# Kernel optimization log

Hardware: AMD Instinct MI355X
Metric: run time of the kernel (lower is better)

## Reference

```python
import jax, jax.numpy as jnp
import numpy as np

DIM = 256
N_PATCHES = 2048
N_HEADS = 8
BATCH = 2


def setup_inputs() -> dict:
    key = jax.random.key(0)
    ks = jax.random.split(key, 8)
    d = DIM
    s = d ** -0.5
    return {
        "x": jax.random.normal(ks[0], (BATCH, N_PATCHES, d), dtype=jnp.float32),
        # weights stored (in_features, out_features) so y = x @ W + b
        "W_qk": jax.random.normal(ks[1], (d, 2 * d), dtype=jnp.float32) * s,
        "W_v": jax.random.normal(ks[2], (d, d), dtype=jnp.float32) * s,
        "W_proj": jax.random.normal(ks[3], (d, d), dtype=jnp.float32) * s,
        "b_proj": jnp.zeros((d,), dtype=jnp.float32),
        "W_pos": jax.random.normal(ks[4], (2, N_HEADS), dtype=jnp.float32) * 0.5,
        "b_pos": jnp.zeros((N_HEADS,), dtype=jnp.float32),
        "gating": jnp.ones((N_HEADS,), dtype=jnp.float32),
    }


def reference(x, W_qk, W_v, W_proj, b_proj, W_pos, b_pos, gating):
    B, N, C = x.shape
    H = gating.shape[0]
    Dh = C // H
    scale = Dh ** -0.5

    # content attention: q @ k^T softmax
    qk = (x @ W_qk).reshape(B, N, 2, H, Dh)
    q = jnp.transpose(qk[:, :, 0], (0, 2, 1, 3))  # [B,H,N,Dh]
    k = jnp.transpose(qk[:, :, 1], (0, 2, 1, 3))
    patch_score = jax.nn.softmax(jnp.einsum("bhnd,bhmd->bhnm", q, k) * scale, axis=-1)

    # positional attention from relative indices (d, |d|) -> per-head score
    idx = jnp.arange(N, dtype=jnp.float32)
    rel = idx[:, None] - idx[None, :]                      # [N,N]
    rel_feat = jnp.stack([rel, jnp.abs(rel)], axis=-1)     # [N,N,2]
    pos = rel_feat @ W_pos + b_pos                         # [N,N,H]
    pos_score = jax.nn.softmax(jnp.transpose(pos, (2, 0, 1)), axis=-1)  # [H,N,N]

    g = jax.nn.sigmoid(gating)[None, :, None, None]        # [1,H,1,1]
    attn = (1.0 - g) * patch_score + g * pos_score[None]   # [B,H,N,N]
    attn = attn / jnp.sum(attn, axis=-1, keepdims=True)

    v = jnp.transpose((x @ W_v).reshape(B, N, H, Dh), (0, 2, 1, 3))  # [B,H,N,Dh]
    out = jnp.einsum("bhnm,bhmd->bhnd", attn, v)
    out = jnp.transpose(out, (0, 2, 1, 3)).reshape(B, N, C)
    return out @ W_proj + b_proj
```

## Files before the change

kernel.cpp:

```cpp
#include <hip/hip_runtime.h>
#include <hip/hip_bf16.h>

#define DIM 256
#define NP 2048
#define NH 8
#define BATCH 2
#define DH 32

typedef __attribute__((ext_vector_type(8))) short bshort8;
typedef __attribute__((ext_vector_type(4))) short bshort4;
typedef __attribute__((ext_vector_type(4))) float f32x4;

#define LOG2E 1.44269504f
#define QSCALE (0.17677669529663687f * LOG2E)

union U16B { uint4 u; bshort8 s8; __hip_bfloat16 h[8]; };
union U8B  { uint2 u; bshort4 s4; __hip_bfloat16 h[4]; };

__device__ __forceinline__ float fexp2(float x) { return __builtin_amdgcn_exp2f(x); }
__device__ __forceinline__ unsigned packbf(float hi, float lo) {
    return __builtin_amdgcn_perm(__float_as_uint(hi), __float_as_uint(lo), 0x07060302u);
}

__device__ __forceinline__ int lds_addr(int row, int colg) {
    return row * 256 + (((colg ^ (row & 7)) & 31) << 3);
}

__global__ __launch_bounds__(256) void prep_kernel(
    const float* __restrict__ Wqk,
    const float* __restrict__ Wv,
    const float* __restrict__ Wproj,
    __hip_bfloat16* __restrict__ WT) {
    const int t = threadIdx.x;
    const int blk = blockIdx.x;
    __shared__ float ts[64][65];
    const int ct = blk >> 2, k0 = (blk & 3) * 64;
    const int c0 = ct * 64;
    const float* src; int ldw, cs0; float scl = 1.0f;
    if (ct < 8)       { src = Wqk;   ldw = 512; cs0 = c0;      if (ct < 4) scl = QSCALE; }
    else if (ct < 12) { src = Wv;    ldw = 256; cs0 = c0 - 512; }
    else              { src = Wproj; ldw = 256; cs0 = c0 - 768; }
    const int cc = t & 63, tq = t >> 6;
#pragma unroll
    for (int j = 0; j < 16; j++) {
        int kk = tq * 16 + j;
        ts[kk][cc] = src[(size_t)(k0 + kk) * ldw + cs0 + cc];
    }
    __syncthreads();
    const int kk2 = t & 63;
#pragma unroll
    for (int j = 0; j < 16; j++) {
        int cc2 = tq * 16 + j;
        WT[(size_t)(c0 + cc2) * 256 + k0 + kk2] = __float2bfloat16(ts[kk2][cc2] * scl);
    }
}

__global__ __launch_bounds__(256) void qkv_mfma(
    const float* __restrict__ x,
    const __hip_bfloat16* __restrict__ WT,
    __hip_bfloat16* __restrict__ q,
    __hip_bfloat16* __restrict__ k,
    __hip_bfloat16* __restrict__ vT) {
    __shared__ __align__(16) __hip_bfloat16 As[64 * 256];
    __shared__ __align__(16) __hip_bfloat16 Bs[64 * 256];
    const int t = threadIdx.x, lane = t & 63, wvid = t >> 6;
    const int l15 = lane & 15, l4 = lane >> 4;
    const int m0 = blockIdx.x * 64;
    const int nb0 = blockIdx.y * 64;
    const int nc = nb0 + wvid * 16 + l15;

#pragma unroll
    for (int j = 0; j < 8; j++) {
        const int flat = j * 2048 + t * 8;
        const int row = flat >> 8, colg = (flat >> 3) & 31;
        float4 f0 = *(const float4*)(x + (size_t)m0 * 256 + flat);
        float4 f1 = *(const float4*)(x + (size_t)m0 * 256 + flat + 4);
        U16B a;
        a.h[0] = __float2bfloat16(f0.x); a.h[1] = __float2bfloat16(f0.y);
        a.h[2] = __float2bfloat16(f0.z); a.h[3] = __float2bfloat16(f0.w);
        a.h[4] = __float2bfloat16(f1.x); a.h[5] = __float2bfloat16(f1.y);
        a.h[6] = __float2bfloat16(f1.z); a.h[7] = __float2bfloat16(f1.w);
        *(uint4*)&As[lds_addr(row, colg)] = a.u;
        *(uint4*)&Bs[lds_addr(row, colg)] = *(const uint4*)(WT + (size_t)nb0 * 256 + flat);
    }
    __syncthreads();

    f32x4 acc[4] = {{0.f,0.f,0.f,0.f},{0.f,0.f,0.f,0.f},{0.f,0.f,0.f,0.f},{0.f,0.f,0.f,0.f}};
#pragma unroll
    for (int kk = 0; kk < 8; kk++) {
        const int colg = kk * 4 + l4;
        U16B bw; bw.u = *(const uint4*)&Bs[lds_addr(wvid * 16 + l15, colg)];
#pragma unroll
        for (int mt = 0; mt < 4; mt++) {
            U16B ax; ax.u = *(const uint4*)&As[lds_addr(mt * 16 + l15, colg)];
            acc[mt] = __builtin_amdgcn_mfma_f32_16x16x32_bf16(ax.s8, bw.s8, acc[mt], 0, 0, 0);
        }
    }

    if (nb0 < 256) {
        const int h = nc >> 5, d = nc & 31;
#pragma unroll
        for (int mt = 0; mt < 4; mt++)
#pragma unroll
            for (int r = 0; r < 4; r++) {
                int tok = m0 + mt * 16 + l4 * 4 + r;
                int b = tok >> 11, n = tok & (NP - 1);
                q[((size_t)(b * NH + h) * NP + n) * DH + d] = __float2bfloat16(acc[mt][r]);
            }
    } else if (nb0 < 512) {
        const int c = nc - 256, h = c >> 5, d = c & 31;
#pragma unroll
        for (int mt = 0; mt < 4; mt++)
#pragma unroll
            for (int r = 0; r < 4; r++) {
                int tok = m0 + mt * 16 + l4 * 4 + r;
                int b = tok >> 11, n = tok & (NP - 1);
                k[((size_t)(b * NH + h) * NP + n) * DH + d] = __float2bfloat16(acc[mt][r]);
            }
    } else {
        const int c = nc - 512;
        const int b = m0 >> 11;
#pragma unroll
        for (int mt = 0; mt < 4; mt++) {
            int tokn = (m0 & (NP - 1)) + mt * 16 + l4 * 4;
            U8B vv;
#pragma unroll
            for (int r = 0; r < 4; r++) vv.h[r] = __float2bfloat16(acc[mt][r]);
            *(uint2*)(vT + (size_t)(b * 256 + c) * NP + tokn) = vv.u;
        }
    }
}

__global__ __launch_bounds__(512, 4) void attn_kernel(
    const __hip_bfloat16* __restrict__ qg,
    const __hip_bfloat16* __restrict__ kg,
    const __hip_bfloat16* __restrict__ vTg,
    const float* __restrict__ Wpos,
    const float* __restrict__ bpos,
    const float* __restrict__ gating,
    __hip_bfloat16* __restrict__ ao) {
    __shared__ __align__(16) __hip_bfloat16 Kt[2][2][64][40];
    __shared__ __align__(16) __hip_bfloat16 Vt[2][2][32][68];
    __shared__ float cmb[4][2][32][16];
    __shared__ float cls[4][2][16];

    const int t = threadIdx.x;
    const int lane = t & 63, wvid = t >> 6;
    const int l15 = lane & 15, l4 = lane >> 4;
    const int qt = wvid & 3, kh = wvid >> 2;
    const int bh = blockIdx.x >> 5, qb = blockIdx.x & 31;
    const int h = bh & (NH - 1), b = bh >> 3;
    const int q0 = qb * 64 + qt * 16;
    const int myq = q0 + l15;

    const int st_ = t & 255;
    const int kstart = kh * 1024;
    const __hip_bfloat16* kptr = kg + (size_t)bh * NP * DH + (size_t)(kstart + (st_ >> 2)) * DH + (st_ & 3) * 8;
    const __hip_bfloat16* vptr = vTg + ((size_t)bh * DH + (st_ >> 3)) * NP + kstart + (st_ & 7) * 8;

    uint4 kreg = *(const uint4*)kptr;
    uint4 vreg = *(const uint4*)vptr;
    *(uint4*)&Kt[kh][0][st_ >> 2][(st_ & 3) * 8] = kreg;
    *(uint2*)&Vt[kh][0][st_ >> 3][(st_ & 7) * 8]     = make_uint2(vreg.x, vreg.y);
    *(uint2*)&Vt[kh][0][st_ >> 3][(st_ & 7) * 8 + 4] = make_uint2(vreg.z, vreg.w);

    const float w0 = Wpos[h] * LOG2E;
    const float w1 = Wpos[NH + h] * LOG2E;
    const float g = 1.0f / (1.0f + __expf(-gating[h]));
    const float nf = (float)myq;
    const float pmax = fmaxf(0.f, fmaxf((w0 + w1) * nf, (w1 - w0) * (2047.0f - nf)));
    const float npmax = -pmax;
    const float rA = fexp2(-(w0 + w1));
    const float rB = fexp2(w1 - w0);

    U16B qv;
    qv.u = *(const uint4*)(qg + ((size_t)bh * NP + myq) * DH + l4 * 8);

    __syncthreads();

    f32x4 os0 = {0.f,0.f,0.f,0.f}, os1 = {0.f,0.f,0.f,0.f};
    f32x4 op0 = {0.f,0.f,0.f,0.f}, op1 = {0.f,0.f,0.f,0.f};
    float ls = 0.f, lp = 0.f;

    for (int it = 0; it < 16; ++it) {
        const int cur = it & 1, nxt = cur ^ 1;

        if (it < 15) {
            kreg = *(const uint4*)(kptr + (size_t)(it + 1) * 64 * DH);
            vreg = *(const uint4*)(vptr + (it + 1) * 64);
        }

        f32x4 st4[4];
#pragma unroll
        for (int kt = 0; kt < 4; kt++) {
            U16B kf; kf.u = *(const uint4*)&Kt[kh][cur][kt * 16 + l15][l4 * 8];
            st4[kt] = __builtin_amdgcn_mfma_f32_16x16x32_bf16(
                kf.s8, qv.s8, (f32x4){0.f,0.f,0.f,0.f}, 0, 0, 0);
        }

        U8B vfr[8];
#pragma unroll
        for (int vh = 0; vh < 2; vh++)
#pragma unroll
            for (int kt = 0; kt < 4; kt++)
                vfr[vh * 4 + kt].u = *(const uint2*)&Vt[kh][cur][vh * 16 + l15][kt * 16 + l4 * 4];

        const int kb0 = kstart + it * 64;
#pragma unroll
        for (int kt = 0; kt < 4; kt++) {
            float es0 = fexp2(st4[kt][0]), es1 = fexp2(st4[kt][1]);
            float es2 = fexp2(st4[kt][2]), es3 = fexp2(st4[kt][3]);
            ls += (es0 + es1) + (es2 + es3);
            const float d0 = nf - (float)(kb0 + kt * 16 + l4 * 4);
            float ep0 = fexp2(fmaf(w1, fabsf(d0), fmaf(w0, d0, npmax)));
            float ep1 = ep0 * ((d0 >= 1.f) ? rA : rB);
            float ep2 = ep1 * ((d0 >= 2.f) ? rA : rB);
            float ep3 = ep2 * ((d0 >= 3.f) ? rA : rB);
            lp += (ep0 + ep1) + (ep2 + ep3);
            U8B pc, pp;
            pc.u.x = packbf(es1, es0); pc.u.y = packbf(es3, es2);
            pp.u.x = packbf(ep1, ep0); pp.u.y = packbf(ep3, ep2);
            os0 = __builtin_amdgcn_mfma_f32_16x16x16bf16_1k(vfr[kt].s4,     pc.s4, os0, 0, 0, 0);
            os1 = __builtin_amdgcn_mfma_f32_16x16x16bf16_1k(vfr[4 + kt].s4, pc.s4, os1, 0, 0, 0);
            op0 = __builtin_amdgcn_mfma_f32_16x16x16bf16_1k(vfr[kt].s4,     pp.s4, op0, 0, 0, 0);
            op1 = __builtin_amdgcn_mfma_f32_16x16x16bf16_1k(vfr[4 + kt].s4, pp.s4, op1, 0, 0, 0);
        }

        if (it < 15) {
            *(uint4*)&Kt[kh][nxt][st_ >> 2][(st_ & 3) * 8] = kreg;
            *(uint2*)&Vt[kh][nxt][st_ >> 3][(st_ & 7) * 8]     = make_uint2(vreg.x, vreg.y);
            *(uint2*)&Vt[kh][nxt][st_ >> 3][(st_ & 7) * 8 + 4] = make_uint2(vreg.z, vreg.w);
        }
        __syncthreads();
    }

    ls += __shfl_xor(ls, 16, 64); ls += __shfl_xor(ls, 32, 64);
    lp += __shfl_xor(lp, 16, 64); lp += __shfl_xor(lp, 32, 64);

    if (kh == 1) {
#pragma unroll
        for (int r = 0; r < 4; r++) {
            cmb[qt][0][l4 * 4 + r][l15]      = os0[r];
            cmb[qt][0][16 + l4 * 4 + r][l15] = os1[r];
            cmb[qt][1][l4 * 4 + r][l15]      = op0[r];
            cmb[qt][1][16 + l4 * 4 + r][l15] = op1[r];
        }
        if (l4 == 0) { cls[qt][0][l15] = ls; cls[qt][1][l15] = lp; }
    }
    __syncthreads();
    if (kh == 0) {
        ls += cls[qt][0][l15]; lp += cls[qt][1][l15];
        const float cs = (1.0f - g) / ls;
        const float cp = g / lp;
        const size_t orow = ((size_t)b * NP + myq) * DIM + h * DH;
        U8B o0, o1;
#pragma unroll
        for (int r = 0; r < 4; r++) {
            o0.h[r] = __float2bfloat16(cs * (os0[r] + cmb[qt][0][l4 * 4 + r][l15]) +
                                       cp * (op0[r] + cmb[qt][1][l4 * 4 + r][l15]));
            o1.h[r] = __float2bfloat16(cs * (os1[r] + cmb[qt][0][16 + l4 * 4 + r][l15]) +
                                       cp * (op1[r] + cmb[qt][1][16 + l4 * 4 + r][l15]));
        }
        *(uint2*)(ao + orow + l4 * 4)      = o0.u;
        *(uint2*)(ao + orow + 16 + l4 * 4) = o1.u;
    }
}

__global__ __launch_bounds__(256) void proj_mfma(
    const __hip_bfloat16* __restrict__ ao,
    const __hip_bfloat16* __restrict__ WT,
    const float* __restrict__ bias,
    float* __restrict__ out) {
    __shared__ __align__(16) __hip_bfloat16 As[64 * 256];
    __shared__ __align__(16) __hip_bfloat16 Bs[64 * 256];
    const int t = threadIdx.x, lane = t & 63, wvid = t >> 6;
    const int l15 = lane & 15, l4 = lane >> 4;
    const int m0 = blockIdx.x * 64;
    const int nb0 = blockIdx.y * 64;
    const int nc = nb0 + wvid * 16 + l15;

#pragma unroll
    for (int j = 0; j < 8; j++) {
        const int flat = j * 2048 + t * 8;
        const int row = flat >> 8, colg = (flat >> 3) & 31;
        *(uint4*)&As[lds_addr(row, colg)] = *(const uint4*)(ao + (size_t)m0 * 256 + flat);
        *(uint4*)&Bs[lds_addr(row, colg)] = *(const uint4*)(WT + (size_t)(768 + nb0) * 256 + flat);
    }
    __syncthreads();

    f32x4 acc[4] = {{0.f,0.f,0.f,0.f},{0.f,0.f,0.f,0.f},{0.f,0.f,0.f,0.f},{0.f,0.f,0.f,0.f}};
#pragma unroll
    for (int kk = 0; kk < 8; kk++) {
        const int colg = kk * 4 + l4;
        U16B bw; bw.u = *(const uint4*)&Bs[lds_addr(wvid * 16 + l15, colg)];
#pragma unroll
        for (int mt = 0; mt < 4; mt++) {
            U16B ax; ax.u = *(const uint4*)&As[lds_addr(mt * 16 + l15, colg)];
            acc[mt] = __builtin_amdgcn_mfma_f32_16x16x32_bf16(ax.s8, bw.s8, acc[mt], 0, 0, 0);
        }
    }

    const float bb = bias[nc];
#pragma unroll
    for (int mt = 0; mt < 4; mt++)
#pragma unroll
        for (int r = 0; r < 4; r++) {
            int tok = m0 + mt * 16 + l4 * 4 + r;
            out[(size_t)tok * 256 + nc] = acc[mt][r] + bb;
        }
}

extern "C" void kernel_launch(void* const* d_in, const int* in_sizes, int n_in,
                              void* d_out, int out_size, void* d_ws, size_t ws_size,
                              hipStream_t stream) {
    const float* x      = (const float*)d_in[0];
    const float* Wqk    = (const float*)d_in[1];
    const float* Wv     = (const float*)d_in[2];
    const float* Wproj  = (const float*)d_in[3];
    const float* bproj  = (const float*)d_in[4];
    const float* Wpos   = (const float*)d_in[5];
    const float* bpos   = (const float*)d_in[6];
    const float* gating = (const float*)d_in[7];
    float* out = (float*)d_out;

    const size_t nElem = (size_t)BATCH * NP * DIM;
    char* w = (char*)d_ws;
    __hip_bfloat16* WT = (__hip_bfloat16*)w;
    __hip_bfloat16* q  = WT + 262144;
    __hip_bfloat16* k  = q + nElem;
    __hip_bfloat16* vT = k + nElem;
    __hip_bfloat16* ao = vT + nElem;

    prep_kernel<<<64, 256, 0, stream>>>(Wqk, Wv, Wproj, WT);
    qkv_mfma<<<dim3(64, 12), 256, 0, stream>>>(x, WT, q, k, vT);
    attn_kernel<<<BATCH * NH * (NP / 64), 512, 0, stream>>>(q, k, vT, Wpos, bpos, gating, ao);
    proj_mfma<<<dim3(64, 4), 256, 0, stream>>>(ao, WT, bproj, out);
}
```

Before: 107.4 us.

## Pre-convert x to bf16, use direct global-to-LDS loads, and relayout q and V

x is now converted to bf16 once in the prep kernel, and both GEMM kernels stage their tiles with global_load_lds so data goes straight from global memory to LDS with the swizzle applied through the address. q is stored transposed, like V, which makes the qkv epilogue write vectors, while the attention kernel now reads q with eight strided scalar loads. The V LDS tile is padded and permuted so each lane gets its four MFMA fragments with two 16-byte reads instead of eight 8-byte reads. The cost is an extra bf16 copy of x in workspace plus the strided q gather.

```diff
diff --git a/kernel.cpp b/kernel.cpp
--- a/kernel.cpp
+++ b/kernel.cpp
@@ -14,7 +14,7 @@
 #define LOG2E 1.44269504f
 #define QSCALE (0.17677669529663687f * LOG2E)
 
-union U16B { uint4 u; bshort8 s8; __hip_bfloat16 h[8]; };
+union U16B { uint4 u; bshort8 s8; bshort4 s4x[2]; __hip_bfloat16 h[8]; };
 union U8B  { uint2 u; bshort4 s4; __hip_bfloat16 h[4]; };
 
 __device__ __forceinline__ float fexp2(float x) { return __builtin_amdgcn_exp2f(x); }
@@ -24,15 +24,36 @@
 
 __device__ __forceinline__ int lds_addr(int row, int colg) {
     return row * 256 + (((colg ^ (row & 7)) & 31) << 3);
+}
+
+__device__ __forceinline__ void gl16(const void* g, void* l) {
+    __builtin_amdgcn_global_load_lds(
+        (const __attribute__((address_space(1))) void*)g,
+        (__attribute__((address_space(3))) void*)l, 16, 0, 0);
 }
 
 __global__ __launch_bounds__(256) void prep_kernel(
     const float* __restrict__ Wqk,
     const float* __restrict__ Wv,
     const float* __restrict__ Wproj,
-    __hip_bfloat16* __restrict__ WT) {
+    const float* __restrict__ x,
+    __hip_bfloat16* __restrict__ WT,
+    __hip_bfloat16* __restrict__ xb) {
     const int t = threadIdx.x;
     const int blk = blockIdx.x;
+    if (blk >= 64) {
+        const int base = (blk - 64) * 256 + t;
+#pragma unroll
+        for (int i = 0; i < 16; i++) {
+            const int idx = base + i * 16384;
+            float4 f = *(const float4*)(x + (size_t)idx * 4);
+            U8B a;
+            a.h[0] = __float2bfloat16(f.x); a.h[1] = __float2bfloat16(f.y);
+            a.h[2] = __float2bfloat16(f.z); a.h[3] = __float2bfloat16(f.w);
+            *(uint2*)(xb + (size_t)idx * 4) = a.u;
+        }
+        return;
+    }
     __shared__ float ts[64][65];
     const int ct = blk >> 2, k0 = (blk & 3) * 64;
     const int c0 = ct * 64;
@@ -56,9 +77,9 @@
 }
 
 __global__ __launch_bounds__(256) void qkv_mfma(
-    const float* __restrict__ x,
+    const __hip_bfloat16* __restrict__ xb,
     const __hip_bfloat16* __restrict__ WT,
-    __hip_bfloat16* __restrict__ q,
+    __hip_bfloat16* __restrict__ qT,
     __hip_bfloat16* __restrict__ k,
     __hip_bfloat16* __restrict__ vT) {
     __shared__ __align__(16) __hip_bfloat16 As[64 * 256];
@@ -69,19 +90,14 @@
     const int nb0 = blockIdx.y * 64;
     const int nc = nb0 + wvid * 16 + l15;
 
+    const int lrow = lane >> 5, lcg = lane & 31;
 #pragma unroll
     for (int j = 0; j < 8; j++) {
-        const int flat = j * 2048 + t * 8;
-        const int row = flat >> 8, colg = (flat >> 3) & 31;
-        float4 f0 = *(const float4*)(x + (size_t)m0 * 256 + flat);
-        float4 f1 = *(const float4*)(x + (size_t)m0 * 256 + flat + 4);
-        U16B a;
-        a.h[0] = __float2bfloat16(f0.x); a.h[1] = __float2bfloat16(f0.y);
-        a.h[2] = __float2bfloat16(f0.z); a.h[3] = __float2bfloat16(f0.w);
-        a.h[4] = __float2bfloat16(f1.x); a.h[5] = __float2bfloat16(f1.y);
-        a.h[6] = __float2bfloat16(f1.z); a.h[7] = __float2bfloat16(f1.w);
-        *(uint4*)&As[lds_addr(row, colg)] = a.u;
-        *(uint4*)&Bs[lds_addr(row, colg)] = *(const uint4*)(WT + (size_t)nb0 * 256 + flat);
+        const int r0 = j * 8 + wvid * 2;
+        const int row = r0 + lrow;
+        const int cgs = (lcg ^ (row & 7)) & 31;
+        gl16(xb + (((size_t)(m0 + row)) << 8) + cgs * 8, (char*)As + r0 * 512);
+        gl16(WT + (((size_t)(nb0 + row)) << 8) + cgs * 8, (char*)Bs + r0 * 512);
     }
     __syncthreads();
 
@@ -98,15 +114,16 @@
     }
 
     if (nb0 < 256) {
-        const int h = nc >> 5, d = nc & 31;
-#pragma unroll
-        for (int mt = 0; mt < 4; mt++)
-#pragma unroll
-            for (int r = 0; r < 4; r++) {
-                int tok = m0 + mt * 16 + l4 * 4 + r;
-                int b = tok >> 11, n = tok & (NP - 1);
-                q[((size_t)(b * NH + h) * NP + n) * DH + d] = __float2bfloat16(acc[mt][r]);
-            }
+        const int c = nc;
+        const int b = m0 >> 11;
+#pragma unroll
+        for (int mt = 0; mt < 4; mt++) {
+            int tokn = (m0 & (NP - 1)) + mt * 16 + l4 * 4;
+            U8B vv;
+#pragma unroll
+            for (int r = 0; r < 4; r++) vv.h[r] = __float2bfloat16(acc[mt][r]);
+            *(uint2*)(qT + (size_t)(b * 256 + c) * NP + tokn) = vv.u;
+        }
     } else if (nb0 < 512) {
         const int c = nc - 256, h = c >> 5, d = c & 31;
 #pragma unroll
@@ -140,7 +157,7 @@
     const float* __restrict__ gating,
     __hip_bfloat16* __restrict__ ao) {
     __shared__ __align__(16) __hip_bfloat16 Kt[2][2][64][40];
-    __shared__ __align__(16) __hip_bfloat16 Vt[2][2][32][68];
+    __shared__ __align__(16) __hip_bfloat16 Vt[2][2][32][72];
     __shared__ float cmb[4][2][32][16];
     __shared__ float cls[4][2][16];
 
@@ -158,11 +175,15 @@
     const __hip_bfloat16* kptr = kg + (size_t)bh * NP * DH + (size_t)(kstart + (st_ >> 2)) * DH + (st_ & 3) * 8;
     const __hip_bfloat16* vptr = vTg + ((size_t)bh * DH + (st_ >> 3)) * NP + kstart + (st_ & 7) * 8;
 
+    const int vd = st_ >> 3, vs = st_ & 7;
+    const int vc0 = ((2 * vs) & 3) * 16 + (vs >> 1) * 4;
+    const int vc1 = ((2 * vs + 1) & 3) * 16 + (vs >> 1) * 4;
+
     uint4 kreg = *(const uint4*)kptr;
     uint4 vreg = *(const uint4*)vptr;
     *(uint4*)&Kt[kh][0][st_ >> 2][(st_ & 3) * 8] = kreg;
-    *(uint2*)&Vt[kh][0][st_ >> 3][(st_ & 7) * 8]     = make_uint2(vreg.x, vreg.y);
-    *(uint2*)&Vt[kh][0][st_ >> 3][(st_ & 7) * 8 + 4] = make_uint2(vreg.z, vreg.w);
+    *(uint2*)&Vt[kh][0][vd][vc0] = make_uint2(vreg.x, vreg.y);
+    *(uint2*)&Vt[kh][0][vd][vc1] = make_uint2(vreg.z, vreg.w);
 
     const float w0 = Wpos[h] * LOG2E;
     const float w1 = Wpos[NH + h] * LOG2E;
@@ -174,7 +195,9 @@
     const float rB = fexp2(w1 - w0);
 
     U16B qv;
-    qv.u = *(const uint4*)(qg + ((size_t)bh * NP + myq) * DH + l4 * 8);
+#pragma unroll
+    for (int j = 0; j < 8; j++)
+        qv.h[j] = qg[((size_t)bh * DH + l4 * 8 + j) * NP + myq];
 
     __syncthreads();
 
@@ -198,16 +221,21 @@
                 kf.s8, qv.s8, (f32x4){0.f,0.f,0.f,0.f}, 0, 0, 0);
         }
 
-        U8B vfr[8];
-#pragma unroll
-        for (int vh = 0; vh < 2; vh++)
-#pragma unroll
-            for (int kt = 0; kt < 4; kt++)
-                vfr[vh * 4 + kt].u = *(const uint2*)&Vt[kh][cur][vh * 16 + l15][kt * 16 + l4 * 4];
+        U16B va0, va1, vb0, vb1;
+        {
+            const __hip_bfloat16* v0 = &Vt[kh][cur][l15][l4 * 16];
+            const __hip_bfloat16* v1 = &Vt[kh][cur][16 + l15][l4 * 16];
+            va0.u = *(const uint4*)v0;
+            va1.u = *(const uint4*)(v0 + 8);
+            vb0.u = *(const uint4*)v1;
+            vb1.u = *(const uint4*)(v1 + 8);
+        }
 
         const int kb0 = kstart + it * 64;
 #pragma unroll
         for (int kt = 0; kt < 4; kt++) {
+            const bshort4 fa = (kt < 2) ? va0.s4x[kt & 1] : va1.s4x[kt & 1];
+            const bshort4 fb = (kt < 2) ? vb0.s4x[kt & 1] : vb1.s4x[kt & 1];
             float es0 = fexp2(st4[kt][0]), es1 = fexp2(st4[kt][1]);
             float es2 = fexp2(st4[kt][2]), es3 = fexp2(st4[kt][3]);
             ls += (es0 + es1) + (es2 + es3);
@@ -220,16 +248,16 @@
             U8B pc, pp;
             pc.u.x = packbf(es1, es0); pc.u.y = packbf(es3, es2);
             pp.u.x = packbf(ep1, ep0); pp.u.y = packbf(ep3, ep2);
-            os0 = __builtin_amdgcn_mfma_f32_16x16x16bf16_1k(vfr[kt].s4,     pc.s4, os0, 0, 0, 0);
-            os1 = __builtin_amdgcn_mfma_f32_16x16x16bf16_1k(vfr[4 + kt].s4, pc.s4, os1, 0, 0, 0);
-            op0 = __builtin_amdgcn_mfma_f32_16x16x16bf16_1k(vfr[kt].s4,     pp.s4, op0, 0, 0, 0);
-            op1 = __builtin_amdgcn_mfma_f32_16x16x16bf16_1k(vfr[4 + kt].s4, pp.s4, op1, 0, 0, 0);
+            os0 = __builtin_amdgcn_mfma_f32_16x16x16bf16_1k(fa, pc.s4, os0, 0, 0, 0);
+            os1 = __builtin_amdgcn_mfma_f32_16x16x16bf16_1k(fb, pc.s4, os1, 0, 0, 0);
+            op0 = __builtin_amdgcn_mfma_f32_16x16x16bf16_1k(fa, pp.s4, op0, 0, 0, 0);
+            op1 = __builtin_amdgcn_mfma_f32_16x16x16bf16_1k(fb, pp.s4, op1, 0, 0, 0);
         }
 
         if (it < 15) {
             *(uint4*)&Kt[kh][nxt][st_ >> 2][(st_ & 3) * 8] = kreg;
-            *(uint2*)&Vt[kh][nxt][st_ >> 3][(st_ & 7) * 8]     = make_uint2(vreg.x, vreg.y);
-            *(uint2*)&Vt[kh][nxt][st_ >> 3][(st_ & 7) * 8 + 4] = make_uint2(vreg.z, vreg.w);
+            *(uint2*)&Vt[kh][nxt][vd][vc0] = make_uint2(vreg.x, vreg.y);
+            *(uint2*)&Vt[kh][nxt][vd][vc1] = make_uint2(vreg.z, vreg.w);
         }
         __syncthreads();
     }
@@ -279,12 +307,14 @@
     const int nb0 = blockIdx.y * 64;
     const int nc = nb0 + wvid * 16 + l15;
 
+    const int lrow = lane >> 5, lcg = lane & 31;
 #pragma unroll
     for (int j = 0; j < 8; j++) {
-        const int flat = j * 2048 + t * 8;
-        const int row = flat >> 8, colg = (flat >> 3) & 31;
-        *(uint4*)&As[lds_addr(row, colg)] = *(const uint4*)(ao + (size_t)m0 * 256 + flat);
-        *(uint4*)&Bs[lds_addr(row, colg)] = *(const uint4*)(WT + (size_t)(768 + nb0) * 256 + flat);
+        const int r0 = j * 8 + wvid * 2;
+        const int row = r0 + lrow;
+        const int cgs = (lcg ^ (row & 7)) & 31;
+        gl16(ao + (((size_t)(m0 + row)) << 8) + cgs * 8, (char*)As + r0 * 512);
+        gl16(WT + (((size_t)(768 + nb0 + row)) << 8) + cgs * 8, (char*)Bs + r0 * 512);
     }
     __syncthreads();
 
@@ -326,13 +356,14 @@
     const size_t nElem = (size_t)BATCH * NP * DIM;
     char* w = (char*)d_ws;
     __hip_bfloat16* WT = (__hip_bfloat16*)w;
-    __hip_bfloat16* q  = WT + 262144;
-    __hip_bfloat16* k  = q + nElem;
+    __hip_bfloat16* qT = WT + 262144;
+    __hip_bfloat16* k  = qT + nElem;
     __hip_bfloat16* vT = k + nElem;
     __hip_bfloat16* ao = vT + nElem;
-
-    prep_kernel<<<64, 256, 0, stream>>>(Wqk, Wv, Wproj, WT);
-    qkv_mfma<<<dim3(64, 12), 256, 0, stream>>>(x, WT, q, k, vT);
-    attn_kernel<<<BATCH * NH * (NP / 64), 512, 0, stream>>>(q, k, vT, Wpos, bpos, gating, ao);
+    __hip_bfloat16* xb = ao + nElem;
+
+    prep_kernel<<<128, 256, 0, stream>>>(Wqk, Wv, Wproj, x, WT, xb);
+    qkv_mfma<<<dim3(64, 12), 256, 0, stream>>>(xb, WT, qT, k, vT);
+    attn_kernel<<<BATCH * NH * (NP / 64), 512, 0, stream>>>(qT, k, vT, Wpos, bpos, gating, ao);
     proj_mfma<<<dim3(64, 4), 256, 0, stream>>>(ao, WT, bproj, out);
 }
```

Measured after the change: 107.8 us. Within noise of the previous version (+0.3%).
